# Optimization experiments

Hardware: AMD Instinct MI355X
Metric: run time of the kernel (lower is better)

The kernel has to match this reference:

```python
import jax, jax.numpy as jnp
import numpy as np
import math

N, L, C, H = 16, 2048, 512, 8
D = C // H  # head channels = 64


def setup_inputs() -> dict:
    key = jax.random.key(0)
    ks = jax.random.split(key, 18)
    s = 1.0 / math.sqrt(C)
    sd = 1.0 / math.sqrt(D)
    return {
        "x_q": jax.random.normal(ks[0], (N, L, C), jnp.float32),
        "x_kv": jax.random.normal(ks[1], (N, L, C), jnp.float32),
        "Wq": jax.random.normal(ks[2], (C, C), jnp.float32) * s,
        "bq": jax.random.normal(ks[3], (C,), jnp.float32) * s,
        "wqa": jax.random.normal(ks[4], (D,), jnp.float32) * sd,
        "bqa": jax.random.normal(ks[5], (1,), jnp.float32) * sd,
        "Wk": jax.random.normal(ks[6], (C, C), jnp.float32) * s,
        "bk": jax.random.normal(ks[7], (C,), jnp.float32) * s,
        "wka": jax.random.normal(ks[8], (D,), jnp.float32) * sd,
        "bka": jax.random.normal(ks[9], (1,), jnp.float32) * sd,
        "Wv": jax.random.normal(ks[10], (C, C), jnp.float32) * s,
        "bv": jax.random.normal(ks[11], (C,), jnp.float32) * s,
        "Wt": jax.random.normal(ks[12], (D, D), jnp.float32) * sd,
        "bt": jax.random.normal(ks[13], (D,), jnp.float32) * sd,
        "Wp": jax.random.normal(ks[14], (C, C), jnp.float32) * s,
        "bp": jax.random.normal(ks[15], (C,), jnp.float32) * s,
    }


def _separate_heads(x):
    # (N, L, C) -> (N, H, L, D)
    n, l, _ = x.shape
    return x.reshape(n, l, H, D).transpose(0, 2, 1, 3)


def reference(x_q, x_kv, Wq, bq, wqa, bqa, Wk, bk, wka, bka, Wv, bv, Wt, bt, Wp, bp):
    inv_sqrt_d = 1.0 / math.sqrt(D)

    # Query projection (torch Linear: y = x @ W.T + b), dropout is identity (eval)
    q = _separate_heads(x_q @ Wq.T + bq)  # (N,H,L,D)
    # Additive pooling of queries over L
    q_score = (jnp.einsum("nhld,d->nhl", q, wqa) + bqa[0]) * inv_sqrt_d
    q_weight = jax.nn.softmax(q_score, axis=-1)  # (N,H,L)
    pooled_q = jnp.einsum("nhl,nhld->nhd", q_weight, q)[:, :, None, :]  # (N,H,1,D)

    # Key projection, gated by pooled query
    k = _separate_heads(x_kv @ Wk.T + bk)  # (N,H,L,D)
    kq = k * pooled_q
    k_score = (jnp.einsum("nhld,d->nhl", kq, wka) + bka[0]) * inv_sqrt_d
    k_weight = jax.nn.softmax(k_score, axis=-1)
    pooled_k = jnp.einsum("nhl,nhld->nhd", k_weight, k)[:, :, None, :]  # (N,H,1,D)

    # Value projection, gated by pooled key, then per-head transform
    v = _separate_heads(x_kv @ Wv.T + bv)  # (N,H,L,D)
    kv = jnp.einsum("nhld,ed->nhle", v * pooled_k, Wt) + bt

    out = kv + q  # (N,H,L,D)
    out = out.transpose(0, 2, 1, 3).reshape(out.shape[0], out.shape[2], C)  # group heads
    return out @ Wp.T + bp
```

## Files before the change

### kernel.cpp

```cpp
#include <hip/hip_runtime.h>
#include <hip/hip_bf16.h>
#include <math.h>

#define NB 16
#define LL 2048
#define CC 512
#define HH 8
#define MM (NB*LL)

typedef __attribute__((ext_vector_type(8))) short bf16x8;
typedef __attribute__((ext_vector_type(4))) float f32x4;
typedef __attribute__((ext_vector_type(8))) unsigned short u16x8;

__device__ inline unsigned short f2bf(float x) {
    __hip_bfloat16 b = __float2bfloat16(x);
    return __builtin_bit_cast(unsigned short, b);
}
__device__ inline float bf2f(unsigned short u) {
    __hip_bfloat16 b = __builtin_bit_cast(__hip_bfloat16, u);
    return __bfloat162float(b);
}
__device__ inline void split2(float x, unsigned short& h, unsigned short& l) {
    unsigned short hh = f2bf(x);
    float fh = bf2f(hh);
    h = hh;
    l = f2bf(x - fh);
}

__global__ __launch_bounds__(256)
void prep_kernel(const float* __restrict__ Wq, const float* __restrict__ Wk,
                 const float* __restrict__ Wv, const float* __restrict__ Wt,
                 const float* __restrict__ bt, const float* __restrict__ Wp,
                 const float* __restrict__ bp,
                 unsigned short* __restrict__ Bqh, unsigned short* __restrict__ Bql,
                 unsigned short* __restrict__ Bkh, unsigned short* __restrict__ Bkl,
                 unsigned short* __restrict__ Bvh, unsigned short* __restrict__ Bvl,
                 unsigned short* __restrict__ WBh, unsigned short* __restrict__ WBl,
                 float* __restrict__ cvec)
{
    const int t = blockIdx.x * 256 + threadIdx.x;
    const int c = t >> 10;
    const int k = t & 1023;
    float val;
    if (k < 512) {
        const int h = k >> 6, d = k & 63;
        float s = 0.f;
        #pragma unroll 8
        for (int e = 0; e < 64; ++e) s += Wt[e * 64 + d] * Wp[c * CC + h * 64 + e];
        val = s;
    } else {
        val = Wp[c * CC + (k - 512)];
    }
    unsigned short hh, ll;
    split2(val, hh, ll);
    const size_t pw = (((size_t)(c >> 7) * 128 + (k >> 3)) * 128 + (c & 127)) * 8 + (k & 7);
    WBh[pw] = hh; WBl[pw] = ll;
    if (k < 512) {
        const size_t pq = (((size_t)(c >> 7) * 64 + (k >> 3)) * 128 + (c & 127)) * 8 + (k & 7);
        split2(Wq[c * CC + k], hh, ll); Bqh[pq] = hh; Bql[pq] = ll;
        split2(Wk[c * CC + k], hh, ll); Bkh[pq] = hh; Bkl[pq] = ll;
        split2(Wv[c * CC + k], hh, ll); Bvh[pq] = hh; Bvl[pq] = ll;
    }
    if (k == 0) {
        float cv = bp[c];
        for (int j = 0; j < 512; ++j) cv += bt[j & 63] * Wp[c * CC + j];
        cvec[c] = cv;
    }
}

template<int KT1, int KT2, bool G1>
__global__ __launch_bounds__(256)
void gemm_f32a(const float* __restrict__ A1, const float* __restrict__ A2,
               const float* __restrict__ gate,
               const unsigned short* __restrict__ Bh, const unsigned short* __restrict__ Bl,
               const float* __restrict__ bias, float* __restrict__ out)
{
    constexpr int KT = KT1 + KT2;
    __shared__ __align__(16) unsigned short sAh[4096], sAl[4096], sBh[4096], sBl[4096];
    const int tid = threadIdx.x;
    const int nt = blockIdx.x;
    const int mt = blockIdx.y;
    const int n0 = nt * 128, m0 = mt * 128;
    const int l = tid & 63, w = tid >> 6;
    const int wm = w >> 1, wn = w & 1;
    const int so = w * 1024 + (l << 4);
    const int smp = mt >> 4;

    f32x4 acc[4][4] = {};

    float4 pa0, pa1, pa2, pa3;
    uint4 rbh0, rbh1, rbl0, rbl1;

    auto loadTile = [&](int kt) {
        const float* Asrc; int k0; bool g;
        if (KT2 == 0 || kt < KT1) { Asrc = A1; k0 = kt * 32; g = G1; }
        else                      { Asrc = A2; k0 = (kt - KT1) * 32; g = false; }
        {
            const int row = tid & 127, kp = tid >> 7;
            const float* p = Asrc + (size_t)(m0 + row) * CC + k0 + kp * 8;
            float4 a0 = *(const float4*)p, a1 = *(const float4*)(p + 4);
            if (g) {
                const float* gp = gate + smp * CC + k0 + kp * 8;
                const float4 g0 = *(const float4*)gp, g1 = *(const float4*)(gp + 4);
                a0.x *= g0.x; a0.y *= g0.y; a0.z *= g0.z; a0.w *= g0.w;
                a1.x *= g1.x; a1.y *= g1.y; a1.z *= g1.z; a1.w *= g1.w;
            }
            pa0 = a0; pa1 = a1;
        }
        {
            const int idx = 256 + tid;
            const int row = idx & 127, kp = idx >> 7;
            const float* p = Asrc + (size_t)(m0 + row) * CC + k0 + kp * 8;
            float4 a0 = *(const float4*)p, a1 = *(const float4*)(p + 4);
            if (g) {
                const float* gp = gate + smp * CC + k0 + kp * 8;
                const float4 g0 = *(const float4*)gp, g1 = *(const float4*)(gp + 4);
                a0.x *= g0.x; a0.y *= g0.y; a0.z *= g0.z; a0.w *= g0.w;
                a1.x *= g1.x; a1.y *= g1.y; a1.z *= g1.z; a1.w *= g1.w;
            }
            pa2 = a0; pa3 = a1;
        }
        const size_t ob = ((size_t)nt * KT + kt) * 8192;
        const char* bh = (const char*)Bh + ob;
        const char* bl = (const char*)Bl + ob;
        rbh0 = *(const uint4*)(bh + so); rbh1 = *(const uint4*)(bh + so + 4096);
        rbl0 = *(const uint4*)(bl + so); rbl1 = *(const uint4*)(bl + so + 4096);
    };

    auto storeTile = [&]() {
        {
            const int row = tid & 127, kp = tid >> 7;
            float x[8];
            *(float4*)&x[0] = pa0; *(float4*)&x[4] = pa1;
            u16x8 hv, lv;
            #pragma unroll
            for (int j = 0; j < 8; ++j) { unsigned short h, lo; split2(x[j], h, lo); hv[j] = h; lv[j] = lo; }
            *(u16x8*)&sAh[(kp * 128 + row) * 8] = hv;
            *(u16x8*)&sAl[(kp * 128 + row) * 8] = lv;
        }
        {
            const int idx = 256 + tid;
            const int row = idx & 127, kp = idx >> 7;
            float x[8];
            *(float4*)&x[0] = pa2; *(float4*)&x[4] = pa3;
            u16x8 hv, lv;
            #pragma unroll
            for (int j = 0; j < 8; ++j) { unsigned short h, lo; split2(x[j], h, lo); hv[j] = h; lv[j] = lo; }
            *(u16x8*)&sAh[(kp * 128 + row) * 8] = hv;
            *(u16x8*)&sAl[(kp * 128 + row) * 8] = lv;
        }
        *(uint4*)((char*)sBh + so) = rbh0; *(uint4*)((char*)sBh + so + 4096) = rbh1;
        *(uint4*)((char*)sBl + so) = rbl0; *(uint4*)((char*)sBl + so + 4096) = rbl1;
    };

    loadTile(0);

    for (int kt = 0; kt < KT; ++kt) {
        __syncthreads();
        storeTile();
        __syncthreads();
        if (kt + 1 < KT) loadTile(kt + 1);

        const int g = l >> 4;
        const int rA = wm * 64 + (l & 15);
        const int rB = wn * 64 + (l & 15);
        const bf16x8* vAh = (const bf16x8*)sAh; const bf16x8* vAl = (const bf16x8*)sAl;
        const bf16x8* vBh = (const bf16x8*)sBh; const bf16x8* vBl = (const bf16x8*)sBl;
        bf16x8 ah[4], al[4], bh[4], bl[4];
        #pragma unroll
        for (int f = 0; f < 4; ++f) {
            ah[f] = vAh[g * 128 + rA + f * 16];
            al[f] = vAl[g * 128 + rA + f * 16];
            bh[f] = vBh[g * 128 + rB + f * 16];
            bl[f] = vBl[g * 128 + rB + f * 16];
        }
        #pragma unroll
        for (int i = 0; i < 4; ++i)
            #pragma unroll
            for (int j = 0; j < 4; ++j) {
                acc[i][j] = __builtin_amdgcn_mfma_f32_16x16x32_bf16(ah[i], bh[j], acc[i][j], 0, 0, 0);
                acc[i][j] = __builtin_amdgcn_mfma_f32_16x16x32_bf16(ah[i], bl[j], acc[i][j], 0, 0, 0);
                acc[i][j] = __builtin_amdgcn_mfma_f32_16x16x32_bf16(al[i], bh[j], acc[i][j], 0, 0, 0);
            }
    }

    const int rowb = (l >> 4) * 4, colb = l & 15;
    #pragma unroll
    for (int j = 0; j < 4; ++j) {
        const int c = n0 + wn * 64 + j * 16 + colb;
        const float bv = bias[c];
        #pragma unroll
        for (int i = 0; i < 4; ++i) {
            const int r = m0 + wm * 64 + i * 16 + rowb;
            #pragma unroll
            for (int e = 0; e < 4; ++e)
                out[(size_t)(r + e) * CC + c] = acc[i][j][e] + bv;
        }
    }
}

__global__ __launch_bounds__(256)
void pool_scores(const float* __restrict__ src, const float* __restrict__ wvec,
                 const float* __restrict__ bscal, float* __restrict__ scores, int modeK)
{
    const int nh = blockIdx.x, chunk = blockIdx.y;
    const int n = nh >> 3, h = nh & 7;
    const int tid = threadIdx.x;
    const int wave = tid >> 6, lane = tid & 63;
    const int sub = lane >> 4;
    const int c4 = (lane & 15) * 4;
    const float b = bscal[0];
    const float* wv = modeK ? (wvec + nh * 64) : wvec;
    const float4 w4 = *(const float4*)&wv[c4];
    const float* base = src + (size_t)n * LL * CC + h * 64;
    const int l0 = chunk * 128 + wave * 32;
    #pragma unroll
    for (int it = 0; it < 8; ++it) {
        const int ll = l0 + it * 4 + sub;
        const float4 x = *(const float4*)&base[(size_t)ll * CC + c4];
        float s = x.x * w4.x + x.y * w4.y + x.z * w4.z + x.w * w4.w;
        s += __shfl_xor(s, 1, 64);
        s += __shfl_xor(s, 2, 64);
        s += __shfl_xor(s, 4, 64);
        s += __shfl_xor(s, 8, 64);
        if ((lane & 15) == 0) scores[nh * LL + ll] = (s + b) * 0.125f;
    }
}

__global__ __launch_bounds__(256)
void pool_softmax(float* __restrict__ scores)
{
    __shared__ float sc[2048];
    __shared__ float red[8];
    const int nh = blockIdx.x;
    const int tid = threadIdx.x;
    const int wave = tid >> 6, lane = tid & 63;
    float mx = -INFINITY;
    for (int i = tid; i < LL; i += 256) {
        const float v = scores[nh * LL + i];
        sc[i] = v;
        mx = fmaxf(mx, v);
    }
    #pragma unroll
    for (int off = 32; off > 0; off >>= 1) mx = fmaxf(mx, __shfl_xor(mx, off, 64));
    if (lane == 0) red[wave] = mx;
    __syncthreads();
    mx = fmaxf(fmaxf(red[0], red[1]), fmaxf(red[2], red[3]));
    float e[8], sum = 0.f;
    #pragma unroll
    for (int j = 0; j < 8; ++j) {
        e[j] = expf(sc[tid + j * 256] - mx);
        sum += e[j];
    }
    #pragma unroll
    for (int off = 32; off > 0; off >>= 1) sum += __shfl_xor(sum, off, 64);
    if (lane == 0) red[4 + wave] = sum;
    __syncthreads();
    const float inv = 1.f / (red[4] + red[5] + red[6] + red[7]);
    #pragma unroll
    for (int j = 0; j < 8; ++j) scores[nh * LL + tid + j * 256] = e[j] * inv;
}

__global__ __launch_bounds__(256)
void pool_wsum(const float* __restrict__ src, const float* __restrict__ scores,
               float* __restrict__ partials)
{
    __shared__ float sm[256];
    const int nh = blockIdx.x, chunk = blockIdx.y;
    const int n = nh >> 3, h = nh & 7;
    const int tid = threadIdx.x;
    const int wave = tid >> 6, d = tid & 63;
    const float* base = src + (size_t)n * LL * CC + h * 64;
    const int l0 = chunk * 128 + wave * 32;
    float acc = 0.f;
    for (int r = 0; r < 32; ++r) {
        const int ll = l0 + r;
        acc += scores[nh * LL + ll] * base[(size_t)ll * CC + d];
    }
    sm[tid] = acc;
    __syncthreads();
    if (wave == 0) {
        const float p = sm[d] + sm[64 + d] + sm[128 + d] + sm[192 + d];
        partials[((size_t)nh * 16 + chunk) * 64 + d] = p;
    }
}

__global__ __launch_bounds__(64)
void pool_combine(const float* __restrict__ partials, const float* __restrict__ postmul,
                  float* __restrict__ pooled)
{
    const int nh = blockIdx.x, d = threadIdx.x;
    float p = 0.f;
    #pragma unroll
    for (int c = 0; c < 16; ++c) p += partials[((size_t)nh * 16 + c) * 64 + d];
    if (postmul) p *= postmul[d];
    pooled[nh * 64 + d] = p;
}

#define OFF_BQH   0ull
#define OFF_BQL   524288ull
#define OFF_BKH   1048576ull
#define OFF_BKL   1572864ull
#define OFF_BVH   2097152ull
#define OFF_BVL   2621440ull
#define OFF_WBH   3145728ull
#define OFF_WBL   4194304ull
#define OFF_CVEC  5242880ull
#define OFF_GQ    5259264ull
#define OFF_PK    5292032ull
#define OFF_PART  5324800ull
#define OFF_SC    0ull
#define OFF_QBUF  6291456ull
#define OFF_KV    73400320ull

extern "C" void kernel_launch(void* const* d_in, const int* in_sizes, int n_in,
                              void* d_out, int out_size, void* d_ws, size_t ws_size,
                              hipStream_t stream) {
    const float* x_q  = (const float*)d_in[0];
    const float* x_kv = (const float*)d_in[1];
    const float* Wq   = (const float*)d_in[2];
    const float* bq   = (const float*)d_in[3];
    const float* wqa  = (const float*)d_in[4];
    const float* bqa  = (const float*)d_in[5];
    const float* Wk   = (const float*)d_in[6];
    const float* bk   = (const float*)d_in[7];
    const float* wka  = (const float*)d_in[8];
    const float* bka  = (const float*)d_in[9];
    const float* Wv   = (const float*)d_in[10];
    const float* bv   = (const float*)d_in[11];
    const float* Wt   = (const float*)d_in[12];
    const float* bt   = (const float*)d_in[13];
    const float* Wp   = (const float*)d_in[14];
    const float* bp   = (const float*)d_in[15];
    float* out = (float*)d_out;
    char* ws = (char*)d_ws;

    unsigned short* Bqh = (unsigned short*)(ws + OFF_BQH);
    unsigned short* Bql = (unsigned short*)(ws + OFF_BQL);
    unsigned short* Bkh = (unsigned short*)(ws + OFF_BKH);
    unsigned short* Bkl = (unsigned short*)(ws + OFF_BKL);
    unsigned short* Bvh = (unsigned short*)(ws + OFF_BVH);
    unsigned short* Bvl = (unsigned short*)(ws + OFF_BVL);
    unsigned short* WBh = (unsigned short*)(ws + OFF_WBH);
    unsigned short* WBl = (unsigned short*)(ws + OFF_WBL);
    float* cvec = (float*)(ws + OFF_CVEC);
    float* gq   = (float*)(ws + OFF_GQ);
    float* pk   = (float*)(ws + OFF_PK);
    float* part = (float*)(ws + OFF_PART);
    float* sc   = (float*)(ws + OFF_SC);
    float* qbuf  = (float*)(ws + OFF_QBUF);
    float* kvbuf = (float*)(ws + OFF_KV);

    const dim3 ggrid(4, 256);
    const dim3 pgrid(NB * HH, 16);

    prep_kernel<<<2048, 256, 0, stream>>>(Wq, Wk, Wv, Wt, bt, Wp, bp,
                                          Bqh, Bql, Bkh, Bkl, Bvh, Bvl, WBh, WBl, cvec);
    gemm_f32a<16, 0, false><<<ggrid, 256, 0, stream>>>(x_q, nullptr, nullptr, Bqh, Bql, bq, qbuf);
    pool_scores<<<pgrid, 256, 0, stream>>>(qbuf, wqa, bqa, sc, 0);
    pool_softmax<<<NB * HH, 256, 0, stream>>>(sc);
    pool_wsum<<<pgrid, 256, 0, stream>>>(qbuf, sc, part);
    pool_combine<<<NB * HH, 64, 0, stream>>>(part, wka, gq);
    gemm_f32a<16, 0, false><<<ggrid, 256, 0, stream>>>(x_kv, nullptr, nullptr, Bkh, Bkl, bk, kvbuf);
    pool_scores<<<pgrid, 256, 0, stream>>>(kvbuf, gq, bka, sc, 1);
    pool_softmax<<<NB * HH, 256, 0, stream>>>(sc);
    pool_wsum<<<pgrid, 256, 0, stream>>>(kvbuf, sc, part);
    pool_combine<<<NB * HH, 64, 0, stream>>>(part, nullptr, pk);
    gemm_f32a<16, 0, false><<<ggrid, 256, 0, stream>>>(x_kv, nullptr, nullptr, Bvh, Bvl, bv, kvbuf);
    gemm_f32a<16, 16, true><<<ggrid, 256, 0, stream>>>(kvbuf, qbuf, pk, WBh, WBl, cvec, out);
}
```

Measured before the change: 587.4 us.

## Widen GEMM tiles to 128x256 with XCD-aware mapping and fuse pooling softmax passes

Each GEMM block now has 512 threads and computes a 128x256 output tile, with blocks remapped so rows stay grouped per XCD. Each A tile is therefore converted to bf16 fewer times across the N dimension, and the B weight layout is changed to a plain k-major interleave. The separate score, softmax and weighted-sum pooling kernels are replaced by an unnormalized exp-accumulate pass plus a combine that divides by the summed exponentials. This removes the score buffer round trip and two launches. The fused form has no max subtraction, so large scores could overflow.

```diff
diff --git a/kernel.cpp b/kernel.cpp
--- a/kernel.cpp
+++ b/kernel.cpp
@@ -53,13 +53,12 @@
     }
     unsigned short hh, ll;
     split2(val, hh, ll);
-    const size_t pw = (((size_t)(c >> 7) * 128 + (k >> 3)) * 128 + (c & 127)) * 8 + (k & 7);
+    const size_t pw = (((size_t)(k >> 3) * 512) + c) * 8 + (k & 7);
     WBh[pw] = hh; WBl[pw] = ll;
     if (k < 512) {
-        const size_t pq = (((size_t)(c >> 7) * 64 + (k >> 3)) * 128 + (c & 127)) * 8 + (k & 7);
-        split2(Wq[c * CC + k], hh, ll); Bqh[pq] = hh; Bql[pq] = ll;
-        split2(Wk[c * CC + k], hh, ll); Bkh[pq] = hh; Bkl[pq] = ll;
-        split2(Wv[c * CC + k], hh, ll); Bvh[pq] = hh; Bvl[pq] = ll;
+        split2(Wq[c * CC + k], hh, ll); Bqh[pw] = hh; Bql[pw] = ll;
+        split2(Wk[c * CC + k], hh, ll); Bkh[pw] = hh; Bkl[pw] = ll;
+        split2(Wv[c * CC + k], hh, ll); Bvh[pw] = hh; Bvl[pw] = ll;
     }
     if (k == 0) {
         float cv = bp[c];
@@ -69,88 +68,65 @@
 }
 
 template<int KT1, int KT2, bool G1>
-__global__ __launch_bounds__(256)
+__global__ __launch_bounds__(512, 4)
 void gemm_f32a(const float* __restrict__ A1, const float* __restrict__ A2,
                const float* __restrict__ gate,
                const unsigned short* __restrict__ Bh, const unsigned short* __restrict__ Bl,
                const float* __restrict__ bias, float* __restrict__ out)
 {
     constexpr int KT = KT1 + KT2;
-    __shared__ __align__(16) unsigned short sAh[4096], sAl[4096], sBh[4096], sBl[4096];
+    __shared__ __align__(16) unsigned short sAh[4096], sAl[4096];
+    __shared__ __align__(16) unsigned short sBh[8192], sBl[8192];
     const int tid = threadIdx.x;
-    const int nt = blockIdx.x;
-    const int mt = blockIdx.y;
-    const int n0 = nt * 128, m0 = mt * 128;
+    const int flat = blockIdx.x;
+    const int xcd = flat & 7, idx = flat >> 3;
+    const int mt = xcd * 32 + (idx >> 1);
+    const int nt = idx & 1;
+    const int n0 = nt * 256, m0 = mt * 128;
     const int l = tid & 63, w = tid >> 6;
-    const int wm = w >> 1, wn = w & 1;
-    const int so = w * 1024 + (l << 4);
+    const int wm = w >> 2, wn = w & 3;
     const int smp = mt >> 4;
 
+    const int arow = tid & 127, akp = tid >> 7;
+    const int bcol = tid & 255, bkp0 = tid >> 8;
+
     f32x4 acc[4][4] = {};
 
-    float4 pa0, pa1, pa2, pa3;
-    uint4 rbh0, rbh1, rbl0, rbl1;
+    float4 pa0, pa1;
+    uint4 pbh0, pbh1, pbl0, pbl1;
 
     auto loadTile = [&](int kt) {
-        const float* Asrc; int k0; bool g;
-        if (KT2 == 0 || kt < KT1) { Asrc = A1; k0 = kt * 32; g = G1; }
-        else                      { Asrc = A2; k0 = (kt - KT1) * 32; g = false; }
-        {
-            const int row = tid & 127, kp = tid >> 7;
-            const float* p = Asrc + (size_t)(m0 + row) * CC + k0 + kp * 8;
-            float4 a0 = *(const float4*)p, a1 = *(const float4*)(p + 4);
-            if (g) {
-                const float* gp = gate + smp * CC + k0 + kp * 8;
-                const float4 g0 = *(const float4*)gp, g1 = *(const float4*)(gp + 4);
-                a0.x *= g0.x; a0.y *= g0.y; a0.z *= g0.z; a0.w *= g0.w;
-                a1.x *= g1.x; a1.y *= g1.y; a1.z *= g1.z; a1.w *= g1.w;
-            }
-            pa0 = a0; pa1 = a1;
+        const float* Asrc; int k0g; bool g;
+        if (KT2 == 0 || kt < KT1) { Asrc = A1; k0g = kt * 32; g = G1; }
+        else                      { Asrc = A2; k0g = (kt - KT1) * 32; g = false; }
+        const float* p = Asrc + (size_t)(m0 + arow) * CC + k0g + akp * 8;
+        float4 a0 = *(const float4*)p, a1 = *(const float4*)(p + 4);
+        if (g) {
+            const float* gp = gate + smp * CC + k0g + akp * 8;
+            const float4 g0 = *(const float4*)gp, g1 = *(const float4*)(gp + 4);
+            a0.x *= g0.x; a0.y *= g0.y; a0.z *= g0.z; a0.w *= g0.w;
+            a1.x *= g1.x; a1.y *= g1.y; a1.z *= g1.z; a1.w *= g1.w;
         }
-        {
-            const int idx = 256 + tid;
-            const int row = idx & 127, kp = idx >> 7;
-            const float* p = Asrc + (size_t)(m0 + row) * CC + k0 + kp * 8;
-            float4 a0 = *(const float4*)p, a1 = *(const float4*)(p + 4);
-            if (g) {
-                const float* gp = gate + smp * CC + k0 + kp * 8;
-                const float4 g0 = *(const float4*)gp, g1 = *(const float4*)(gp + 4);
-                a0.x *= g0.x; a0.y *= g0.y; a0.z *= g0.z; a0.w *= g0.w;
-                a1.x *= g1.x; a1.y *= g1.y; a1.z *= g1.z; a1.w *= g1.w;
-            }
-            pa2 = a0; pa3 = a1;
-        }
-        const size_t ob = ((size_t)nt * KT + kt) * 8192;
-        const char* bh = (const char*)Bh + ob;
-        const char* bl = (const char*)Bl + ob;
-        rbh0 = *(const uint4*)(bh + so); rbh1 = *(const uint4*)(bh + so + 4096);
-        rbl0 = *(const uint4*)(bl + so); rbl1 = *(const uint4*)(bl + so + 4096);
+        pa0 = a0; pa1 = a1;
+        const int kpg = kt * 4;
+        const size_t ob0 = (((size_t)(kpg + bkp0) * 512) + n0 + bcol) * 8;
+        const size_t ob1 = (((size_t)(kpg + bkp0 + 2) * 512) + n0 + bcol) * 8;
+        pbh0 = *(const uint4*)&Bh[ob0]; pbh1 = *(const uint4*)&Bh[ob1];
+        pbl0 = *(const uint4*)&Bl[ob0]; pbl1 = *(const uint4*)&Bl[ob1];
     };
 
     auto storeTile = [&]() {
-        {
-            const int row = tid & 127, kp = tid >> 7;
-            float x[8];
-            *(float4*)&x[0] = pa0; *(float4*)&x[4] = pa1;
-            u16x8 hv, lv;
-            #pragma unroll
-            for (int j = 0; j < 8; ++j) { unsigned short h, lo; split2(x[j], h, lo); hv[j] = h; lv[j] = lo; }
-            *(u16x8*)&sAh[(kp * 128 + row) * 8] = hv;
-            *(u16x8*)&sAl[(kp * 128 + row) * 8] = lv;
-        }
-        {
-            const int idx = 256 + tid;
-            const int row = idx & 127, kp = idx >> 7;
-            float x[8];
-            *(float4*)&x[0] = pa2; *(float4*)&x[4] = pa3;
-            u16x8 hv, lv;
-            #pragma unroll
-            for (int j = 0; j < 8; ++j) { unsigned short h, lo; split2(x[j], h, lo); hv[j] = h; lv[j] = lo; }
-            *(u16x8*)&sAh[(kp * 128 + row) * 8] = hv;
-            *(u16x8*)&sAl[(kp * 128 + row) * 8] = lv;
-        }
-        *(uint4*)((char*)sBh + so) = rbh0; *(uint4*)((char*)sBh + so + 4096) = rbh1;
-        *(uint4*)((char*)sBl + so) = rbl0; *(uint4*)((char*)sBl + so + 4096) = rbl1;
+        float x[8];
+        *(float4*)&x[0] = pa0; *(float4*)&x[4] = pa1;
+        u16x8 hv, lv;
+        #pragma unroll
+        for (int j = 0; j < 8; ++j) { unsigned short h, lo; split2(x[j], h, lo); hv[j] = h; lv[j] = lo; }
+        *(u16x8*)&sAh[(akp * 128 + arow) * 8] = hv;
+        *(u16x8*)&sAl[(akp * 128 + arow) * 8] = lv;
+        *(uint4*)&sBh[(bkp0 * 256 + bcol) * 8] = pbh0;
+        *(uint4*)&sBh[((bkp0 + 2) * 256 + bcol) * 8] = pbh1;
+        *(uint4*)&sBl[(bkp0 * 256 + bcol) * 8] = pbl0;
+        *(uint4*)&sBl[((bkp0 + 2) * 256 + bcol) * 8] = pbl1;
     };
 
     loadTile(0);
@@ -171,8 +147,8 @@
         for (int f = 0; f < 4; ++f) {
             ah[f] = vAh[g * 128 + rA + f * 16];
             al[f] = vAl[g * 128 + rA + f * 16];
-            bh[f] = vBh[g * 128 + rB + f * 16];
-            bl[f] = vBl[g * 128 + rB + f * 16];
+            bh[f] = vBh[g * 256 + rB + f * 16];
+            bl[f] = vBl[g * 256 + rB + f * 16];
         }
         #pragma unroll
         for (int i = 0; i < 4; ++i)
@@ -200,99 +176,60 @@
 }
 
 __global__ __launch_bounds__(256)
-void pool_scores(const float* __restrict__ src, const float* __restrict__ wvec,
-                 const float* __restrict__ bscal, float* __restrict__ scores, int modeK)
+void pool_stage1(const float* __restrict__ src, const float* __restrict__ wvec,
+                 const float* __restrict__ bscal, float* __restrict__ partials,
+                 int modeK)
 {
+    __shared__ float sm[256];
+    __shared__ float se[4];
     const int nh = blockIdx.x, chunk = blockIdx.y;
     const int n = nh >> 3, h = nh & 7;
     const int tid = threadIdx.x;
-    const int wave = tid >> 6, lane = tid & 63;
-    const int sub = lane >> 4;
-    const int c4 = (lane & 15) * 4;
+    const int wave = tid >> 6, d = tid & 63;
+    const float wv = modeK ? wvec[nh * 64 + d] : wvec[d];
     const float b = bscal[0];
-    const float* wv = modeK ? (wvec + nh * 64) : wvec;
-    const float4 w4 = *(const float4*)&wv[c4];
     const float* base = src + (size_t)n * LL * CC + h * 64;
-    const int l0 = chunk * 128 + wave * 32;
-    #pragma unroll
-    for (int it = 0; it < 8; ++it) {
-        const int ll = l0 + it * 4 + sub;
-        const float4 x = *(const float4*)&base[(size_t)ll * CC + c4];
-        float s = x.x * w4.x + x.y * w4.y + x.z * w4.z + x.w * w4.w;
+    float accv = 0.f, acce = 0.f;
+    const int l0 = chunk * 128 + wave;
+    #pragma unroll 4
+    for (int it = 0; it < 32; ++it) {
+        const int ll = l0 + it * 4;
+        const float x = base[(size_t)ll * CC + d];
+        float s = x * wv;
         s += __shfl_xor(s, 1, 64);
         s += __shfl_xor(s, 2, 64);
         s += __shfl_xor(s, 4, 64);
         s += __shfl_xor(s, 8, 64);
-        if ((lane & 15) == 0) scores[nh * LL + ll] = (s + b) * 0.125f;
-    }
-}
-
-__global__ __launch_bounds__(256)
-void pool_softmax(float* __restrict__ scores)
-{
-    __shared__ float sc[2048];
-    __shared__ float red[8];
-    const int nh = blockIdx.x;
-    const int tid = threadIdx.x;
-    const int wave = tid >> 6, lane = tid & 63;
-    float mx = -INFINITY;
-    for (int i = tid; i < LL; i += 256) {
-        const float v = scores[nh * LL + i];
-        sc[i] = v;
-        mx = fmaxf(mx, v);
-    }
-    #pragma unroll
-    for (int off = 32; off > 0; off >>= 1) mx = fmaxf(mx, __shfl_xor(mx, off, 64));
-    if (lane == 0) red[wave] = mx;
-    __syncthreads();
-    mx = fmaxf(fmaxf(red[0], red[1]), fmaxf(red[2], red[3]));
-    float e[8], sum = 0.f;
-    #pragma unroll
-    for (int j = 0; j < 8; ++j) {
-        e[j] = expf(sc[tid + j * 256] - mx);
-        sum += e[j];
-    }
-    #pragma unroll
-    for (int off = 32; off > 0; off >>= 1) sum += __shfl_xor(sum, off, 64);
-    if (lane == 0) red[4 + wave] = sum;
-    __syncthreads();
-    const float inv = 1.f / (red[4] + red[5] + red[6] + red[7]);
-    #pragma unroll
-    for (int j = 0; j < 8; ++j) scores[nh * LL + tid + j * 256] = e[j] * inv;
-}
-
-__global__ __launch_bounds__(256)
-void pool_wsum(const float* __restrict__ src, const float* __restrict__ scores,
-               float* __restrict__ partials)
-{
-    __shared__ float sm[256];
-    const int nh = blockIdx.x, chunk = blockIdx.y;
-    const int n = nh >> 3, h = nh & 7;
-    const int tid = threadIdx.x;
-    const int wave = tid >> 6, d = tid & 63;
-    const float* base = src + (size_t)n * LL * CC + h * 64;
-    const int l0 = chunk * 128 + wave * 32;
-    float acc = 0.f;
-    for (int r = 0; r < 32; ++r) {
-        const int ll = l0 + r;
-        acc += scores[nh * LL + ll] * base[(size_t)ll * CC + d];
-    }
-    sm[tid] = acc;
+        s += __shfl_xor(s, 16, 64);
+        s += __shfl_xor(s, 32, 64);
+        const float e = expf((s + b) * 0.125f);
+        accv += e * x;
+        acce += e;
+    }
+    sm[tid] = accv;
+    if (d == 0) se[wave] = acce;
     __syncthreads();
     if (wave == 0) {
-        const float p = sm[d] + sm[64 + d] + sm[128 + d] + sm[192 + d];
-        partials[((size_t)nh * 16 + chunk) * 64 + d] = p;
+        const float pv = sm[d] + sm[64 + d] + sm[128 + d] + sm[192 + d];
+        float* pr = partials + ((size_t)nh * 16 + chunk) * 65;
+        pr[d] = pv;
+        if (d == 0) pr[64] = se[0] + se[1] + se[2] + se[3];
     }
 }
 
 __global__ __launch_bounds__(64)
-void pool_combine(const float* __restrict__ partials, const float* __restrict__ postmul,
-                  float* __restrict__ pooled)
+void pool_stage2(const float* __restrict__ partials, const float* __restrict__ postmul,
+                 float* __restrict__ pooled)
 {
     const int nh = blockIdx.x, d = threadIdx.x;
-    float p = 0.f;
+    float pv = 0.f, pe = 0.f;
     #pragma unroll
-    for (int c = 0; c < 16; ++c) p += partials[((size_t)nh * 16 + c) * 64 + d];
+    for (int c = 0; c < 16; ++c) {
+        const float* pr = partials + ((size_t)nh * 16 + c) * 65;
+        pv += pr[d];
+        pe += pr[64];
+    }
+    float p = pv / pe;
     if (postmul) p *= postmul[d];
     pooled[nh * 64 + d] = p;
 }
@@ -309,9 +246,8 @@
 #define OFF_GQ    5259264ull
 #define OFF_PK    5292032ull
 #define OFF_PART  5324800ull
-#define OFF_SC    0ull
-#define OFF_QBUF  6291456ull
-#define OFF_KV    73400320ull
+#define OFF_QBUF  8388608ull
+#define OFF_KV    75497472ull
 
 extern "C" void kernel_launch(void* const* d_in, const int* in_sizes, int n_in,
                               void* d_out, int out_size, void* d_ws, size_t ws_size,
@@ -347,25 +283,19 @@
     float* gq   = (float*)(ws + OFF_GQ);
     float* pk   = (float*)(ws + OFF_PK);
     float* part = (float*)(ws + OFF_PART);
-    float* sc   = (float*)(ws + OFF_SC);
     float* qbuf  = (float*)(ws + OFF_QBUF);
     float* kvbuf = (float*)(ws + OFF_KV);
 
-    const dim3 ggrid(4, 256);
     const dim3 pgrid(NB * HH, 16);
 
     prep_kernel<<<2048, 256, 0, stream>>>(Wq, Wk, Wv, Wt, bt, Wp, bp,
                                           Bqh, Bql, Bkh, Bkl, Bvh, Bvl, WBh, WBl, cvec);
-    gemm_f32a<16, 0, false><<<ggrid, 256, 0, stream>>>(x_q, nullptr, nullptr, Bqh, Bql, bq, qbuf);
-    pool_scores<<<pgrid, 256, 0, stream>>>(qbuf, wqa, bqa, sc, 0);
-    pool_softmax<<<NB * HH, 256, 0, stream>>>(sc);
-    pool_wsum<<<pgrid, 256, 0, stream>>>(qbuf, sc, part);
-    pool_combine<<<NB * HH, 64, 0, stream>>>(part, wka, gq);
-    gemm_f32a<16, 0, false><<<ggrid, 256, 0, stream>>>(x_kv, nullptr, nullptr, Bkh, Bkl, bk, kvbuf);
-    pool_scores<<<pgrid, 256, 0, stream>>>(kvbuf, gq, bka, sc, 1);
-    pool_softmax<<<NB * HH, 256, 0, stream>>>(sc);
-    pool_wsum<<<pgrid, 256, 0, stream>>>(kvbuf, sc, part);
-    pool_combine<<<NB * HH, 64, 0, stream>>>(part, nullptr, pk);
-    gemm_f32a<16, 0, false><<<ggrid, 256, 0, stream>>>(x_kv, nullptr, nullptr, Bvh, Bvl, bv, kvbuf);
-    gemm_f32a<16, 16, true><<<ggrid, 256, 0, stream>>>(kvbuf, qbuf, pk, WBh, WBl, cvec, out);
-}
+    gemm_f32a<16, 0, false><<<512, 512, 0, stream>>>(x_q, nullptr, nullptr, Bqh, Bql, bq, qbuf);
+    pool_stage1<<<pgrid, 256, 0, stream>>>(qbuf, wqa, bqa, part, 0);
+    pool_stage2<<<NB * HH, 64, 0, stream>>>(part, wka, gq);
+    gemm_f32a<16, 0, false><<<512, 512, 0, stream>>>(x_kv, nullptr, nullptr, Bkh, Bkl, bk, kvbuf);
+    pool_stage1<<<pgrid, 256, 0, stream>>>(kvbuf, gq, bka, part, 1);
+    pool_stage2<<<NB * HH, 64, 0, stream>>>(part, nullptr, pk);
+    gemm_f32a<16, 0, false><<<512, 512, 0, stream>>>(x_kv, nullptr, nullptr, Bvh, Bvl, bv, kvbuf);
+    gemm_f32a<16, 16, true><<<512, 512, 0, stream>>>(kvbuf, qbuf, pk, WBh, WBl, cvec, out);
+}
```

After: 517.3 us. 1.14x faster.
